# Performance work log

Hardware: AMD Instinct MI355X
Metric: run time of the kernel (lower is better)

## Reference

```python
import jax, jax.numpy as jnp
import numpy as np

D_MODEL = 2048
N_HEADS = 16
D_HEAD = 128
INIT_RANGE = 0.02
EPSILON = -100000.0  # mask fill value from the original module


def setup_inputs() -> dict:
    key = jax.random.key(0)
    ks = jax.random.split(key, 6)
    x = jax.random.normal(ks[0], (2, 2048, D_MODEL), dtype=jnp.float32)
    W_Q = jax.random.normal(ks[1], (N_HEADS, D_MODEL, D_HEAD), dtype=jnp.float32) * INIT_RANGE
    W_K = jax.random.normal(ks[2], (N_HEADS, D_MODEL, D_HEAD), dtype=jnp.float32) * INIT_RANGE
    W_V = jax.random.normal(ks[3], (N_HEADS, D_MODEL, D_HEAD), dtype=jnp.float32) * INIT_RANGE
    W_O = jax.random.normal(ks[4], (N_HEADS, D_HEAD, D_MODEL), dtype=jnp.float32) * INIT_RANGE
    b_Q = jnp.zeros((N_HEADS, D_HEAD), dtype=jnp.float32)
    b_K = jnp.zeros((N_HEADS, D_HEAD), dtype=jnp.float32)
    b_V = jnp.zeros((N_HEADS, D_HEAD), dtype=jnp.float32)
    b_O = jnp.zeros((D_MODEL,), dtype=jnp.float32)
    return {"normalized_resid_pre": x, "W_Q": W_Q, "b_Q": b_Q, "W_K": W_K,
            "b_K": b_K, "W_V": W_V, "b_V": b_V, "W_O": W_O, "b_O": b_O}


def reference(normalized_resid_pre, W_Q, b_Q, W_K, b_K, W_V, b_V, W_O, b_O):
    x = normalized_resid_pre  # [b, s, d_model]
    # per-head projections: [b, s, h, d_head]
    q = jnp.einsum('bsd,hdk->bshk', x, W_Q) + b_Q
    k = jnp.einsum('bsd,hdk->bshk', x, W_K) + b_K
    v = jnp.einsum('bsd,hdk->bshk', x, W_V) + b_V
    # attention scores [b, h, q, k]
    scores = jnp.einsum('bqhk,bshk->bhqs', q, k) / jnp.sqrt(jnp.float32(D_HEAD))
    S = scores.shape[-1]
    causal = jnp.tril(jnp.ones((S, S), dtype=bool))  # True = keep
    scores = jnp.where(causal, scores, jnp.float32(EPSILON))
    pattern = jax.nn.softmax(scores, axis=-1)
    z = jnp.einsum('bhqs,bshk->bqhk', pattern, v)
    attn_out = jnp.einsum('bqhk,hkd->bqd', z, W_O) + b_O
    return attn_out
```

## Files before the change

### kernel.cpp

```cpp
#include <hip/hip_runtime.h>
#include <hip/hip_bf16.h>

typedef unsigned short bfu;
typedef short          bf16x8 __attribute__((ext_vector_type(8)));
typedef float          floatx4 __attribute__((ext_vector_type(4)));
typedef unsigned short bfu4 __attribute__((ext_vector_type(4)));
typedef unsigned int   u32x2 __attribute__((ext_vector_type(2)));

__device__ __forceinline__ bfu f2bf(float f) {
    __hip_bfloat16 h = __float2bfloat16(f);
    return __builtin_bit_cast(unsigned short, h);
}

__device__ __forceinline__ void glds16(const bfu* g, bfu* l) {
    __builtin_amdgcn_global_load_lds(
        (const __attribute__((address_space(1))) unsigned int*)g,
        (__attribute__((address_space(3))) unsigned int*)l, 16, 0, 0);
}

#define BATCH 2
#define SEQ   2048
#define DM    2048
#define NH    16
#define DKH   128
#define SCALE 0.08838834764831845f

__global__ __launch_bounds__(256)
void cvt_x(const float* __restrict__ x, bfu* __restrict__ xb, int n) {
    const int i = (blockIdx.x * 256 + threadIdx.x) * 4;
    if (i >= n) return;
    const float4 v = *(const float4*)(x + i);
    bfu4 p; p[0] = f2bf(v.x); p[1] = f2bf(v.y); p[2] = f2bf(v.z); p[3] = f2bf(v.w);
    *(bfu4*)(xb + i) = p;
}

__global__ __launch_bounds__(256)
void tcvt(const float* __restrict__ in, bfu* __restrict__ out, int R, int C, float s) {
    __shared__ float tile[32][33];
    const int bz = blockIdx.z;
    const float* src = in + (size_t)bz * R * C;
    bfu* dst = out + (size_t)bz * R * C;
    const int c0 = blockIdx.x * 32, r0 = blockIdx.y * 32;
    const int tx = threadIdx.x, ty = threadIdx.y;
    #pragma unroll
    for (int i = 0; i < 4; i++)
        tile[ty + i*8][tx] = src[(size_t)(r0 + ty + i*8) * C + c0 + tx];
    __syncthreads();
    #pragma unroll
    for (int i = 0; i < 4; i++)
        dst[(size_t)(c0 + ty + i*8) * R + r0 + tx] = f2bf(tile[tx][ty + i*8] * s);
}

__global__ __launch_bounds__(256)
void tcvt_qkv(const float* __restrict__ WQ, const float* __restrict__ WK,
              const float* __restrict__ WV,
              bfu* __restrict__ WtQ, bfu* __restrict__ WtK, bfu* __restrict__ WtV) {
    __shared__ float tile[32][33];
    const int p  = blockIdx.z >> 4;
    const int bz = blockIdx.z & 15;
    const float* src = (p == 0) ? WQ : (p == 1) ? WK : WV;
    bfu*         dst = (p == 0) ? WtQ : (p == 1) ? WtK : WtV;
    const float  s   = (p == 0) ? SCALE : 1.0f;
    src += (size_t)bz * DM * DKH;
    dst += (size_t)bz * DM * DKH;
    const int c0 = blockIdx.x * 32, r0 = blockIdx.y * 32;
    const int tx = threadIdx.x, ty = threadIdx.y;
    #pragma unroll
    for (int i = 0; i < 4; i++)
        tile[ty + i*8][tx] = src[(size_t)(r0 + ty + i*8) * DKH + c0 + tx];
    __syncthreads();
    #pragma unroll
    for (int i = 0; i < 4; i++)
        dst[(size_t)(c0 + ty + i*8) * DM + r0 + tx] = f2bf(tile[tx][ty + i*8] * s);
}

__device__ __forceinline__ void stg_half(const bfu* gbase, bfu* slot,
                                         int wave, int lane, int csw) {
    #pragma unroll
    for (int l = 0; l < 2; l++) {
        const int j = l * 8 + wave;
        glds16(gbase + (size_t)((j >> 1) * 16 + (lane >> 2)) * DM
                     + (j & 1) * 32 + csw,
               slot + j * 512);
    }
}

__device__ __forceinline__ void ld_b8(bf16x8 (&bv)[4][2], const bfu* slot, int rdo) {
    #pragma unroll
    for (int n = 0; n < 4; n++)
        #pragma unroll
        for (int ks = 0; ks < 2; ks++)
            bv[n][ks] = *(const bf16x8*)&slot[(n * 2 + ks) * 512 + rdo];
}

__device__ __forceinline__ void ld_a8(bf16x8 (&af)[4][2], const bfu* slot, int rdo) {
    #pragma unroll
    for (int m = 0; m < 4; m++)
        #pragma unroll
        for (int ks = 0; ks < 2; ks++)
            af[m][ks] = *(const bf16x8*)&slot[(m * 2 + ks) * 512 + rdo];
}

template<int MH, int NHALF>
__device__ __forceinline__ void mfma16(floatx4 (&acc)[8][4],
                                       const bf16x8 (&af)[4][2],
                                       const bf16x8 (&bv)[4][2]) {
    __builtin_amdgcn_s_setprio(1);
    #pragma unroll
    for (int m = 0; m < 4; m++)
        #pragma unroll
        for (int n = 0; n < 2; n++)
            #pragma unroll
            for (int ks = 0; ks < 2; ks++)
                acc[MH*4 + m][NHALF*2 + n] =
                    __builtin_amdgcn_mfma_f32_16x16x32_bf16(
                        af[m][ks], bv[NHALF*2 + n][ks],
                        acc[MH*4 + m][NHALF*2 + n], 0, 0, 0);
    __builtin_amdgcn_s_setprio(0);
}

#define BARW()                                                      \
    __builtin_amdgcn_s_barrier();                                   \
    asm volatile("s_waitcnt lgkmcnt(0)" ::: "memory");              \
    __builtin_amdgcn_sched_barrier(0)

__global__ __launch_bounds__(512, 2)
void proj_qkv8(const bfu* __restrict__ xb,
               const bfu* __restrict__ WtQ, const bfu* __restrict__ WtK,
               const bfu* __restrict__ WtV,
               const float* __restrict__ bQ, const float* __restrict__ bK,
               const float* __restrict__ bV,
               bfu* __restrict__ Qall, bfu* __restrict__ Kall, bfu* __restrict__ Vt) {
    __shared__ __align__(16) bfu As[2][2][8192];
    __shared__ __align__(16) bfu Bs[2][2][8192];

    const int p = blockIdx.y >> 3;
    const bfu*   Wt   = (p == 0) ? WtQ : (p == 1) ? WtK : WtV;
    const float* bias = (p == 0) ? bQ  : (p == 1) ? bK  : bV;
    const float  bscale = (p == 0) ? SCALE : 1.0f;

    const int tid  = threadIdx.x;
    const int lane = tid & 63;
    const int wave = tid >> 6;
    const int lrow = lane & 15;
    const int quad = lane >> 4;
    const int wr   = wave >> 2;
    const int wc   = wave & 3;
    const size_t m0 = (size_t)blockIdx.x * 256;
    const int    n0 = (int)(blockIdx.y & 7) * 256;

    const int csw = ((lane & 3) * 8) ^ ((lane & 32) ? 16 : 0);
    const int rdo = lrow * 32 + ((quad * 8) ^ ((lrow & 8) ? 16 : 0));

    const bfu* Ab = xb + m0 * DM;
    const bfu* Bb = Wt + (size_t)n0 * DM;

    floatx4 acc[8][4] = {};
    bf16x8 af[4][2], bv[4][2];

#define STAGE_A(tau, h)                                                     \
    if ((tau) < 32) stg_half(Ab + (size_t)((h) * 128) * DM + (tau) * 64,    \
                             &As[(tau) & 1][h][0], wave, lane, csw)
#define STAGE_B(tau, h)                                                     \
    if ((tau) < 32) stg_half(Bb + (size_t)((h) * 128) * DM + (tau) * 64,    \
                             &Bs[(tau) & 1][h][0], wave, lane, csw)

    STAGE_B(0, 0); STAGE_B(0, 1); STAGE_A(0, 0); STAGE_A(0, 1);
    STAGE_B(1, 0); STAGE_B(1, 1); STAGE_A(1, 0);
    asm volatile("s_waitcnt vmcnt(6)" ::: "memory");
    __builtin_amdgcn_s_barrier();

    #pragma unroll 1
    for (int i = 0; i < 16; i++) {
        const int t0 = 2 * i;
        ld_b8(bv, &Bs[0][wc >> 1][(wc & 1) * 4096], rdo);
        ld_a8(af, &As[0][wr][0], rdo);
        STAGE_A(t0 + 1, 1);
        BARW();
        mfma16<0, 0>(acc, af, bv);
        __builtin_amdgcn_s_barrier();
        STAGE_B(t0 + 2, 0);
        BARW();
        mfma16<0, 1>(acc, af, bv);
        __builtin_amdgcn_s_barrier();
        ld_a8(af, &As[0][wr][4096], rdo);
        STAGE_B(t0 + 2, 1);
        BARW();
        mfma16<1, 0>(acc, af, bv);
        __builtin_amdgcn_s_barrier();
        STAGE_A(t0 + 2, 0);
        BARW();
        mfma16<1, 1>(acc, af, bv);
        if (i == 15) asm volatile("s_waitcnt vmcnt(0)" ::: "memory");
        else         asm volatile("s_waitcnt vmcnt(6)" ::: "memory");
        __builtin_amdgcn_s_barrier();
        ld_b8(bv, &Bs[1][wc >> 1][(wc & 1) * 4096], rdo);
        ld_a8(af, &As[1][wr][0], rdo);
        STAGE_A(t0 + 2, 1);
        BARW();
        mfma16<0, 0>(acc, af, bv);
        __builtin_amdgcn_s_barrier();
        STAGE_B(t0 + 3, 0);
        BARW();
        mfma16<0, 1>(acc, af, bv);
        __builtin_amdgcn_s_barrier();
        ld_a8(af, &As[1][wr][4096], rdo);
        STAGE_B(t0 + 3, 1);
        BARW();
        mfma16<1, 0>(acc, af, bv);
        __builtin_amdgcn_s_barrier();
        STAGE_A(t0 + 3, 0);
        BARW();
        mfma16<1, 1>(acc, af, bv);
        if (i < 15) asm volatile("s_waitcnt vmcnt(6)" ::: "memory");
        __builtin_amdgcn_s_barrier();
    }
#undef STAGE_A
#undef STAGE_B

    if (p < 2) {
        bfu* Out = (p == 0) ? Qall : Kall;
        #pragma unroll
        for (int m = 0; m < 8; m++) {
            #pragma unroll
            for (int n = 0; n < 4; n++) {
                const int gn = n0 + wc * 64 + n * 16 + lrow;
                const float bvv = bias[gn] * bscale;
                #pragma unroll
                for (int r = 0; r < 4; r++) {
                    const size_t gm = m0 + wr * 128 + m * 16 + quad * 4 + r;
                    Out[gm * DM + gn] = f2bf(acc[m][n][r] + bvv);
                }
            }
        }
    } else {
        #pragma unroll
        for (int m = 0; m < 8; m++) {
            #pragma unroll
            for (int n = 0; n < 4; n++) {
                const int gn = n0 + wc * 64 + n * 16 + lrow;
                const float bvv = bias[gn];
                const size_t gm0 = m0 + wr * 128 + m * 16 + quad * 4;
                const int b = (int)(gm0 >> 11), s = (int)(gm0 & 2047);
                bfu4 pk;
                #pragma unroll
                for (int r = 0; r < 4; r++) pk[r] = f2bf(acc[m][n][r] + bvv);
                *(bfu4*)&Vt[((size_t)(b * NH + (gn >> 7)) * DKH + (gn & 127)) * SEQ + s] = pk;
            }
        }
    }
}

__global__ __launch_bounds__(256)
void flash_attn(const bfu* __restrict__ Q, const bfu* __restrict__ K,
                const bfu* __restrict__ Vt, bfu* __restrict__ Z) {
    __shared__ bfu Ks[4][64][32];
    __shared__ bfu Vs[2][128][32];
    __shared__ bfu Ps[4][16][72];

    const int tid  = threadIdx.x;
    const int lane = tid & 63;
    const int wave = tid >> 6;
    const int lrow = lane & 15;
    const int quad = lane >> 4;
    const int hb = blockIdx.x;
    const int h = hb & 15, b = hb >> 4;
    const int qt = 31 - blockIdx.y;
    const int q0w = qt * 64 + wave * 16;
    const int rowb = lane >> 2, colb = (lane & 3) * 8;

    const bfu* Qrow = Q + (size_t)(b * SEQ + q0w + lrow) * DM + h * DKH;
    bf16x8 qf[4];
    #pragma unroll
    for (int kc = 0; kc < 4; kc++)
        qf[kc] = *(const bf16x8*)(Qrow + kc*32 + quad*8);

    floatx4 z[8] = {};
    float l_loc = 0.f;
    const int qg = q0w + lrow;

    const bfu* Kb = K + (size_t)b * SEQ * DM + h * DKH;
    const bfu* Vb = Vt + (size_t)(b * NH + h) * DKH * SEQ;
    const int ntiles = qt + 1;

    for (int it = 0; it < ntiles; it++) {
        const int s0 = it * 64;
        __syncthreads();
        #pragma unroll
        for (int i = 0; i < 8; i++) {
            const int chunk = wave * 8 + i;
            if (chunk < 16) {
                const int kc = chunk >> 2, kg = chunk & 3;
                glds16(Kb + (size_t)(s0 + kg*16 + rowb) * DM + kc*32 + colb,
                       &Ks[kc][kg*16][0]);
            } else {
                const int c2 = chunk - 16;
                const int sh = c2 >> 3, dg = c2 & 7;
                glds16(Vb + (size_t)(dg*16 + rowb) * SEQ + s0 + sh*32 + colb,
                       &Vs[sh][dg*16][0]);
            }
        }
        __syncthreads();

        floatx4 sc[4];
        #pragma unroll
        for (int st = 0; st < 4; st++) {
            floatx4 a = {};
            #pragma unroll
            for (int kc = 0; kc < 4; kc++) {
                bf16x8 kf = *(const bf16x8*)&Ks[kc][st*16 + lrow][quad*8];
                a = __builtin_amdgcn_mfma_f32_16x16x32_bf16(kf, qf[kc], a, 0, 0, 0);
            }
            sc[st] = a;
        }

        #pragma unroll
        for (int st = 0; st < 4; st++) {
            const int sbase = s0 + st*16 + quad*4;
            const float p0 = (sbase + 0 <= qg) ? __expf(sc[st][0]) : 0.f;
            const float p1 = (sbase + 1 <= qg) ? __expf(sc[st][1]) : 0.f;
            const float p2 = (sbase + 2 <= qg) ? __expf(sc[st][2]) : 0.f;
            const float p3 = (sbase + 3 <= qg) ? __expf(sc[st][3]) : 0.f;
            l_loc += (p0 + p1) + (p2 + p3);
            u32x2 pk;
            pk[0] = (unsigned)f2bf(p0) | ((unsigned)f2bf(p1) << 16);
            pk[1] = (unsigned)f2bf(p2) | ((unsigned)f2bf(p3) << 16);
            *(u32x2*)&Ps[wave][lrow][st*16 + quad*4] = pk;
        }

        bf16x8 pf0 = *(const bf16x8*)&Ps[wave][lrow][quad*8];
        bf16x8 pf1 = *(const bf16x8*)&Ps[wave][lrow][32 + quad*8];
        #pragma unroll
        for (int dt = 0; dt < 8; dt++) {
            bf16x8 v0 = *(const bf16x8*)&Vs[0][dt*16 + lrow][quad*8];
            z[dt] = __builtin_amdgcn_mfma_f32_16x16x32_bf16(pf0, v0, z[dt], 0, 0, 0);
            bf16x8 v1 = *(const bf16x8*)&Vs[1][dt*16 + lrow][quad*8];
            z[dt] = __builtin_amdgcn_mfma_f32_16x16x32_bf16(pf1, v1, z[dt], 0, 0, 0);
        }
    }

    float L = l_loc;
    L += __shfl_xor(L, 16);
    L += __shfl_xor(L, 32);
    float inv[4];
    #pragma unroll
    for (int r = 0; r < 4; r++)
        inv[r] = 1.0f / __shfl(L, quad*4 + r, 64);
    #pragma unroll
    for (int dt = 0; dt < 8; dt++) {
        #pragma unroll
        for (int r = 0; r < 4; r++) {
            const int qq = q0w + quad*4 + r;
            const int dk = dt*16 + lrow;
            Z[(size_t)(b * SEQ + qq) * DM + h * DKH + dk] = f2bf(z[dt][r] * inv[r]);
        }
    }
}

__global__ __launch_bounds__(256)
void out_gemm(const bfu* __restrict__ Zb, const bfu* __restrict__ WtO,
              const float* __restrict__ bO, float* out) {
    __shared__ bfu As[128 * 32];
    __shared__ bfu Bs[128 * 32];
    const int tid  = threadIdx.x;
    const int lane = tid & 63;
    const int wave = tid >> 6;
    const int lrow = lane & 15;
    const int quad = lane >> 4;
    const int mw = (wave & 1) * 64;
    const int nw = (wave >> 1) * 64;
    const size_t m0 = (size_t)blockIdx.x * 128;
    const size_t n0 = (size_t)blockIdx.y * 128;
    const int rowb = lane >> 2, colb = (lane & 3) * 8;

    floatx4 acc[4][4] = {};

    for (int k0 = 0; k0 < DM; k0 += 32) {
        __syncthreads();
        #pragma unroll
        for (int i = 0; i < 2; i++) {
            const int rg = wave * 2 + i;
            glds16(Zb  + (m0 + rg*16 + rowb) * DM + k0 + colb, &As[rg * 512]);
            glds16(WtO + (n0 + rg*16 + rowb) * DM + k0 + colb, &Bs[rg * 512]);
        }
        __syncthreads();
        bf16x8 af[4], bfr[4];
        #pragma unroll
        for (int t = 0; t < 4; t++) {
            af[t]  = *(const bf16x8*)&As[(mw + t*16 + lrow) * 32 + quad * 8];
            bfr[t] = *(const bf16x8*)&Bs[(nw + t*16 + lrow) * 32 + quad * 8];
        }
        #pragma unroll
        for (int mt = 0; mt < 4; mt++)
            #pragma unroll
            for (int nt = 0; nt < 4; nt++)
                acc[mt][nt] = __builtin_amdgcn_mfma_f32_16x16x32_bf16(
                                  af[mt], bfr[nt], acc[mt][nt], 0, 0, 0);
    }

    #pragma unroll
    for (int mt = 0; mt < 4; mt++) {
        #pragma unroll
        for (int nt = 0; nt < 4; nt++) {
            const size_t gn = n0 + nw + nt*16 + lrow;
            const float bv = bO[gn];
            #pragma unroll
            for (int r = 0; r < 4; r++) {
                const size_t gm = m0 + mw + mt*16 + quad*4 + r;
                out[gm * DM + gn] = acc[mt][nt][r] + bv;
            }
        }
    }
}

extern "C" void kernel_launch(void* const* d_in, const int* in_sizes, int n_in,
                              void* d_out, int out_size, void* d_ws, size_t ws_size,
                              hipStream_t stream) {
    const float* x  = (const float*)d_in[0];
    const float* WQ = (const float*)d_in[1];
    const float* bQ = (const float*)d_in[2];
    const float* WK = (const float*)d_in[3];
    const float* bK = (const float*)d_in[4];
    const float* WV = (const float*)d_in[5];
    const float* bV = (const float*)d_in[6];
    const float* WO = (const float*)d_in[7];
    const float* bO = (const float*)d_in[8];
    float* out = (float*)d_out;
    bfu* ws  = (bfu*)d_ws;
    bfu* dob = (bfu*)d_out;

    bfu* Qall = ws;
    bfu* Kall = Qall + 8388608;
    bfu* Vt   = Kall + 8388608;
    bfu* Zb   = Vt   + 8388608;
    bfu* WtV  = Zb;
    bfu* xb   = dob;
    bfu* WtQ  = dob + 8388608;
    bfu* WtK  = dob + 12582912;

    const dim3 tb(32, 8, 1);

    cvt_x<<<8192, 256, 0, stream>>>(x, xb, BATCH * SEQ * DM);

    tcvt_qkv<<<dim3(4, 64, 48), tb, 0, stream>>>(WQ, WK, WV, WtQ, WtK, WtV);
    proj_qkv8<<<dim3(16, 24), 512, 0, stream>>>(xb, WtQ, WtK, WtV,
                                                bQ, bK, bV, Qall, Kall, Vt);

    flash_attn<<<dim3(32, 32), 256, 0, stream>>>(Qall, Kall, Vt, Zb);

    tcvt<<<dim3(64, 64, 1), tb, 0, stream>>>(WO, Qall, DM, DM, 1.0f);
    out_gemm<<<dim3(32, 16), 256, 0, stream>>>(Zb, Qall, bO, out);
}
```

Baseline: 376.9 us.

## Split V projection into separate simpler GEMM kernel with smaller tiles

The fused QKV projection kernel is split in two. Q and K keep the 256x256 pipelined kernel, and V now uses a new 128x128-tile kernel with single-buffered LDS staging and a transposed output store. The likely intent is to reduce the transposed-store cost in the big kernel or change tile-count and wave balance (384 blocks becomes 256 + 512). The new V kernel has no software pipelining, no LDS swizzle and a sync every k-step, so it risks being slower than the tuned path.

```diff
diff --git a/kernel.cpp b/kernel.cpp
--- a/kernel.cpp
+++ b/kernel.cpp
@@ -125,18 +125,16 @@
     __builtin_amdgcn_sched_barrier(0)
 
 __global__ __launch_bounds__(512, 2)
-void proj_qkv8(const bfu* __restrict__ xb,
-               const bfu* __restrict__ WtQ, const bfu* __restrict__ WtK,
-               const bfu* __restrict__ WtV,
-               const float* __restrict__ bQ, const float* __restrict__ bK,
-               const float* __restrict__ bV,
-               bfu* __restrict__ Qall, bfu* __restrict__ Kall, bfu* __restrict__ Vt) {
+void proj_qk8(const bfu* __restrict__ xb,
+              const bfu* __restrict__ WtQ, const bfu* __restrict__ WtK,
+              const float* __restrict__ bQ, const float* __restrict__ bK,
+              bfu* __restrict__ Qall, bfu* __restrict__ Kall) {
     __shared__ __align__(16) bfu As[2][2][8192];
     __shared__ __align__(16) bfu Bs[2][2][8192];
 
     const int p = blockIdx.y >> 3;
-    const bfu*   Wt   = (p == 0) ? WtQ : (p == 1) ? WtK : WtV;
-    const float* bias = (p == 0) ? bQ  : (p == 1) ? bK  : bV;
+    const bfu*   Wt   = (p == 0) ? WtQ : WtK;
+    const float* bias = (p == 0) ? bQ  : bK;
     const float  bscale = (p == 0) ? SCALE : 1.0f;
 
     const int tid  = threadIdx.x;
@@ -218,35 +216,76 @@
 #undef STAGE_A
 #undef STAGE_B
 
-    if (p < 2) {
-        bfu* Out = (p == 0) ? Qall : Kall;
-        #pragma unroll
-        for (int m = 0; m < 8; m++) {
-            #pragma unroll
-            for (int n = 0; n < 4; n++) {
-                const int gn = n0 + wc * 64 + n * 16 + lrow;
-                const float bvv = bias[gn] * bscale;
-                #pragma unroll
-                for (int r = 0; r < 4; r++) {
-                    const size_t gm = m0 + wr * 128 + m * 16 + quad * 4 + r;
-                    Out[gm * DM + gn] = f2bf(acc[m][n][r] + bvv);
-                }
+    bfu* Out = (p == 0) ? Qall : Kall;
+    #pragma unroll
+    for (int m = 0; m < 8; m++) {
+        #pragma unroll
+        for (int n = 0; n < 4; n++) {
+            const int gn = n0 + wc * 64 + n * 16 + lrow;
+            const float bvv = bias[gn] * bscale;
+            #pragma unroll
+            for (int r = 0; r < 4; r++) {
+                const size_t gm = m0 + wr * 128 + m * 16 + quad * 4 + r;
+                Out[gm * DM + gn] = f2bf(acc[m][n][r] + bvv);
             }
         }
-    } else {
-        #pragma unroll
-        for (int m = 0; m < 8; m++) {
-            #pragma unroll
-            for (int n = 0; n < 4; n++) {
-                const int gn = n0 + wc * 64 + n * 16 + lrow;
-                const float bvv = bias[gn];
-                const size_t gm0 = m0 + wr * 128 + m * 16 + quad * 4;
-                const int b = (int)(gm0 >> 11), s = (int)(gm0 & 2047);
-                bfu4 pk;
-                #pragma unroll
-                for (int r = 0; r < 4; r++) pk[r] = f2bf(acc[m][n][r] + bvv);
-                *(bfu4*)&Vt[((size_t)(b * NH + (gn >> 7)) * DKH + (gn & 127)) * SEQ + s] = pk;
-            }
+    }
+}
+
+__global__ __launch_bounds__(256)
+void proj_v(const bfu* __restrict__ xb, const bfu* __restrict__ WtV,
+            const float* __restrict__ bV, bfu* __restrict__ Vt) {
+    __shared__ bfu As[128 * 32];
+    __shared__ bfu Bs[128 * 32];
+    const int tid  = threadIdx.x;
+    const int lane = tid & 63;
+    const int wave = tid >> 6;
+    const int lrow = lane & 15;
+    const int quad = lane >> 4;
+    const int mw = (wave & 1) * 64;
+    const int nw = (wave >> 1) * 64;
+    const size_t m0 = (size_t)blockIdx.x * 128;
+    const size_t n0 = (size_t)blockIdx.y * 128;
+    const int rowb = lane >> 2;
+    const int colb = (lane & 3) * 8;
+
+    floatx4 acc[4][4] = {};
+
+    for (int k0 = 0; k0 < DM; k0 += 32) {
+        __syncthreads();
+        #pragma unroll
+        for (int i = 0; i < 2; i++) {
+            const int rg = wave * 2 + i;
+            glds16(xb  + (m0 + rg*16 + rowb) * DM + k0 + colb, &As[rg * 512]);
+            glds16(WtV + (n0 + rg*16 + rowb) * DM + k0 + colb, &Bs[rg * 512]);
+        }
+        __syncthreads();
+        bf16x8 af[4], bfr[4];
+        #pragma unroll
+        for (int t = 0; t < 4; t++) {
+            af[t]  = *(const bf16x8*)&As[(mw + t*16 + lrow) * 32 + quad * 8];
+            bfr[t] = *(const bf16x8*)&Bs[(nw + t*16 + lrow) * 32 + quad * 8];
+        }
+        #pragma unroll
+        for (int mt = 0; mt < 4; mt++)
+            #pragma unroll
+            for (int nt = 0; nt < 4; nt++)
+                acc[mt][nt] = __builtin_amdgcn_mfma_f32_16x16x32_bf16(
+                                  af[mt], bfr[nt], acc[mt][nt], 0, 0, 0);
+    }
+
+    #pragma unroll
+    for (int mt = 0; mt < 4; mt++) {
+        #pragma unroll
+        for (int nt = 0; nt < 4; nt++) {
+            const int nl = (int)n0 + nw + nt*16 + lrow;
+            const float bvv = bV[nl];
+            const size_t gm0 = m0 + mw + mt*16 + quad*4;
+            const int b = (int)(gm0 >> 11), s = (int)(gm0 & 2047);
+            bfu4 pk;
+            #pragma unroll
+            for (int r = 0; r < 4; r++) pk[r] = f2bf(acc[mt][nt][r] + bvv);
+            *(bfu4*)&Vt[((size_t)(b * NH + (nl >> 7)) * DKH + (nl & 127)) * SEQ + s] = pk;
         }
     }
 }
@@ -443,8 +482,9 @@
     cvt_x<<<8192, 256, 0, stream>>>(x, xb, BATCH * SEQ * DM);
 
     tcvt_qkv<<<dim3(4, 64, 48), tb, 0, stream>>>(WQ, WK, WV, WtQ, WtK, WtV);
-    proj_qkv8<<<dim3(16, 24), 512, 0, stream>>>(xb, WtQ, WtK, WtV,
-                                                bQ, bK, bV, Qall, Kall, Vt);
+
+    proj_qk8<<<dim3(16, 16), 512, 0, stream>>>(xb, WtQ, WtK, bQ, bK, Qall, Kall);
+    proj_v<<<dim3(32, 16), 256, 0, stream>>>(xb, WtV, bV, Vt);
 
     flash_attn<<<dim3(32, 32), 256, 0, stream>>>(Qall, Kall, Vt, Zb);
 
```

Result: faster. 364.8 us (-3.2%).
